# Optimization experiments

Hardware: AMD Instinct MI355X
Metric: run time of the kernel (lower is better)

Reference implementation:

```python
import jax, jax.numpy as jnp
import numpy as np

D_MODEL = 1024
HEADS = 16
Q_DIM = 1024
HEAD_DIM = Q_DIM // HEADS


def setup_inputs() -> dict:
    key = jax.random.key(0)
    ks = jax.random.split(key, 9)
    B, S = 2, 2048
    scale = 1.0 / np.sqrt(D_MODEL)
    inp = {
        "embeddings": jax.random.normal(ks[0], (B, S, D_MODEL), dtype=jnp.float32),
        "Wq": jax.random.normal(ks[1], (D_MODEL, Q_DIM), dtype=jnp.float32) * scale,
        "bq": jnp.zeros((Q_DIM,), dtype=jnp.float32),
        "Wk": jax.random.normal(ks[2], (D_MODEL, Q_DIM), dtype=jnp.float32) * scale,
        "bk": jnp.zeros((Q_DIM,), dtype=jnp.float32),
        "Wv": jax.random.normal(ks[3], (D_MODEL, Q_DIM), dtype=jnp.float32) * scale,
        "bv": jnp.zeros((Q_DIM,), dtype=jnp.float32),
        "Wo": jax.random.normal(ks[4], (Q_DIM, D_MODEL), dtype=jnp.float32) * scale,
        "bo": jnp.zeros((D_MODEL,), dtype=jnp.float32),
    }
    return inp


def reference(embeddings, Wq, bq, Wk, bk, Wv, bv, Wo, bo):
    B, S, _ = embeddings.shape
    # projections -> [B, H, S, Dh]
    def proj(W, b):
        x = embeddings @ W + b
        return x.reshape(B, S, HEADS, HEAD_DIM).transpose(0, 2, 1, 3)
    q = proj(Wq, bq)
    k = proj(Wk, bk)
    v = proj(Wv, bv)
    # scores scaled by sqrt(head_dim) as in source (no mask, dropout is no-op)
    scores = jnp.einsum("bhqd,bhkd->bhqk", q, k) / jnp.sqrt(
        jnp.asarray(HEAD_DIM, dtype=q.dtype)
    )
    p = jax.nn.softmax(scores, axis=-1)
    attn = jnp.einsum("bhqk,bhkd->bhqd", p, v)
    attn = attn.transpose(0, 2, 1, 3).reshape(B, S, Q_DIM)
    return attn @ Wo + bo
```

## Files before the change

### kernel.cpp

```cpp
#include <hip/hip_runtime.h>
#include <hip/hip_bf16.h>

#define BB 2
#define SS 2048
#define DMODEL 1024
#define NHEADS 16
#define DHEAD 64
#define MTOT (BB*SS)
#define NQKV 3072
#define QSCALE 0.18033688011112042f

typedef short bh8 __attribute__((ext_vector_type(8)));
typedef float fx4 __attribute__((ext_vector_type(4)));
typedef unsigned int ux2 __attribute__((ext_vector_type(2)));

__device__ __forceinline__ short f2bs(float f) {
    __hip_bfloat16 h = __float2bfloat16(f);
    return *reinterpret_cast<short*>(&h);
}

__device__ __forceinline__ unsigned pk_bf16(float a, float b) {
    __hip_bfloat162 h = __float22bfloat162_rn(make_float2(a, b));
    return *reinterpret_cast<unsigned*>(&h);
}

__device__ __forceinline__ void gload_lds16(const short* g, short* l) {
    __builtin_amdgcn_global_load_lds(
        (const __attribute__((address_space(1))) unsigned int*)g,
        (__attribute__((address_space(3))) unsigned int*)l, 16, 0, 0);
}

__global__ __launch_bounds__(256) void cvt_emb(const float* __restrict__ x,
                                               short* __restrict__ y, int n) {
    int i = (blockIdx.x * 256 + threadIdx.x) * 4;
    if (i + 3 < n) {
        float4 v = *(const float4*)(x + i);
        short4 o;
        o.x = f2bs(v.x); o.y = f2bs(v.y); o.z = f2bs(v.z); o.w = f2bs(v.w);
        *(short4*)(y + i) = o;
    }
}

__global__ __launch_bounds__(256) void transpose_w(
        const float* __restrict__ Wq, const float* __restrict__ Wk,
        const float* __restrict__ Wv, const float* __restrict__ Wo,
        short* __restrict__ Wt_qkv, short* __restrict__ Wot) {
    __shared__ float tile[64][65];
    int z = blockIdx.z;
    const float* src = (z == 0) ? Wq : (z == 1) ? Wk : (z == 2) ? Wv : Wo;
    short* dst = (z == 3) ? Wot : (Wt_qkv + (size_t)z * 1024 * 1024);
    int n0 = blockIdx.x * 64, k0 = blockIdx.y * 64;
    int tx = threadIdx.x, ty = threadIdx.y;
    for (int j = 0; j < 16; j++) {
        int r = ty + j * 4;
        tile[r][tx] = src[(size_t)(k0 + r) * 1024 + n0 + tx];
    }
    __syncthreads();
    for (int j = 0; j < 16; j++) {
        int r = ty + j * 4;
        dst[(size_t)(n0 + r) * 1024 + k0 + tx] = f2bs(tile[tx][r]);
    }
}

template<int BM, int BN, int NN, int MODE>
__global__ __launch_bounds__(256) void gemm_bt_t(
        const short* __restrict__ A, const short* __restrict__ Bt,
        const float* __restrict__ bq, const float* __restrict__ bk,
        const float* __restrict__ bv, const float* __restrict__ bo,
        short* __restrict__ Qout, short* __restrict__ Kout,
        short* __restrict__ Vtout, float* __restrict__ Cout) {
    const int K = 1024;
    constexpr int ROWS = BM + BN;
    constexpr int CPW  = ROWS / 64;
    constexpr int MBK  = MTOT / BM;
    constexpr int STRIP = MBK / 8;
    constexpr int MT = BM / 32, NT = BN / 32;
    __shared__ __align__(16) short S[3][ROWS * 32];

    int tid = threadIdx.x;
    int w = tid >> 6, l = tid & 63, quad = l >> 4, ln = l & 15;
    int wm = w & 1, wn = w >> 1;

    int id = blockIdx.x;
    int xcd = id & 7, local = id >> 3;
    int mi = xcd * STRIP + (local % STRIP);
    int ni = local / STRIP;
    int m0 = mi * BM, n0 = ni * BN;

    const short* gsrc[CPW];
    int loff[CPW];
    #pragma unroll
    for (int j = 0; j < CPW; j++) {
        int r0 = (w * CPW + j) * 16;
        int row = r0 + (l >> 2);
        gsrc[j] = (r0 < BM ? A + (size_t)(m0 + row) * K
                           : Bt + (size_t)(n0 + row - BM) * K) + (l & 3) * 8;
        loff[j] = r0 * 32;
    }

    short *sC = &S[0][0], *sN = &S[1][0], *sN2 = &S[2][0];
    #pragma unroll
    for (int j = 0; j < CPW; j++) gload_lds16(gsrc[j], sC + loff[j]);
    #pragma unroll
    for (int j = 0; j < CPW; j++) gload_lds16(gsrc[j] + 32, sN + loff[j]);

    fx4 acc[MT][NT] = {};
    for (int it = 0; it < 32; ++it) {
        if (it < 31) {
            if constexpr (CPW == 4)
                asm volatile("s_waitcnt vmcnt(4)\n\ts_barrier" ::: "memory");
            else
                asm volatile("s_waitcnt vmcnt(3)\n\ts_barrier" ::: "memory");
        } else {
            asm volatile("s_waitcnt vmcnt(0)\n\ts_barrier" ::: "memory");
        }
        if (it < 30) {
            int k0 = (it + 2) * 32;
            #pragma unroll
            for (int j = 0; j < CPW; j++) gload_lds16(gsrc[j] + k0, sN2 + loff[j]);
        }
        bh8 af[MT], bf[NT];
        #pragma unroll
        for (int mt = 0; mt < MT; mt++)
            af[mt] = *(const bh8*)&sC[(wm * (BM / 2) + mt * 16 + ln) * 32 + quad * 8];
        #pragma unroll
        for (int nt = 0; nt < NT; nt++)
            bf[nt] = *(const bh8*)&sC[(BM + wn * (BN / 2) + nt * 16 + ln) * 32 + quad * 8];
        #pragma unroll
        for (int mt = 0; mt < MT; mt++)
            #pragma unroll
            for (int nt = 0; nt < NT; nt++)
                acc[mt][nt] = __builtin_amdgcn_mfma_f32_16x16x32_bf16(af[mt], bf[nt], acc[mt][nt], 0, 0, 0);
        short* t;
        t = sC; sC = sN; sN = sN2; sN2 = t;
    }

    #pragma unroll
    for (int mt = 0; mt < MT; mt++) {
        #pragma unroll
        for (int nt = 0; nt < NT; nt++) {
            int n = n0 + wn * (BN / 2) + nt * 16 + ln;
            int mbase = m0 + wm * (BM / 2) + mt * 16 + quad * 4;
            #pragma unroll
            for (int r = 0; r < 4; r++) {
                float v = acc[mt][nt][r];
                int m = mbase + r;
                if constexpr (MODE == 0) {
                    int which = n >> 10, nn = n & 1023, h = nn >> 6, d = nn & 63;
                    float bias = (which == 0) ? bq[nn] : (which == 1) ? bk[nn] : bv[nn];
                    v += bias;
                    int b = m >> 11, s = m & 2047;
                    if (which == 0)
                        Qout[(((size_t)(b * 16 + h) * 2048) + s) * 64 + d] = f2bs(v * QSCALE);
                    else if (which == 1)
                        Kout[(((size_t)(b * 16 + h) * 2048) + s) * 64 + d] = f2bs(v);
                    else
                        Vtout[((size_t)(b * 16 + h) * 64 + d) * 2048 + s] = f2bs(v);
                } else {
                    Cout[(size_t)m * 1024 + n] = v + bo[n];
                }
            }
        }
    }
}

__global__ __launch_bounds__(256, 4) void flash_attn(
        const short* __restrict__ Q, const short* __restrict__ Kg,
        const short* __restrict__ Vt, short* __restrict__ Ctx) {
    __shared__ __align__(16) short SH[16384];

    int tid = threadIdx.x;
    int w = tid >> 6, l = tid & 63, quad = l >> 4, ln = l & 15;
    int id = blockIdx.x;
    int xcd = id & 7, local = id >> 3;
    int bh = xcd * 4 + (local & 3);
    int qx = local >> 2;
    int qblk = qx * 64 + w * 16;
    int b = bh >> 4, h = bh & 15;
    const short* Qb = Q  + (size_t)bh * 2048 * 64;
    const short* Kb = Kg + (size_t)bh * 2048 * 64;
    const short* Vb = Vt + (size_t)bh * 64 * 2048;
    int swz = ln & 7;

    bh8 qf[2];
    #pragma unroll
    for (int c = 0; c < 2; c++)
        qf[c] = *(const bh8*)&Qb[(size_t)(qblk + ln) * 64 + c * 32 + quad * 8];

    const short* srcK[2]; const short* srcV[2]; int dstoff[2];
    #pragma unroll
    for (int j = 0; j < 2; j++) {
        int c = w * 2 + j;
        int row = c * 8 + (l >> 3);
        int pg = (l & 7) ^ (row & 7);
        srcK[j] = Kb + row * 64 + pg * 8;
        srcV[j] = Vb + (size_t)row * 2048 + pg * 8;
        dstoff[j] = c * 512;
    }

    #pragma unroll
    for (int j = 0; j < 2; j++) {
        gload_lds16(srcK[j], SH + dstoff[j]);
        gload_lds16(srcV[j], SH + 8192 + dstoff[j]);
    }

    fx4 o[4] = {};
    float lpart = 0.f;

    for (int it = 0; it < 32; ++it) {
        int koff = (it & 1) ? 4096 : 0;
        asm volatile("s_waitcnt vmcnt(0) lgkmcnt(0)\n\ts_barrier" ::: "memory");
        if (it < 31) {
            int noff = koff ^ 4096;
            int kg = (it + 1) * 4096, vg = (it + 1) * 64;
            #pragma unroll
            for (int j = 0; j < 2; j++) {
                gload_lds16(srcK[j] + kg, SH + noff + dstoff[j]);
                gload_lds16(srcV[j] + vg, SH + 8192 + noff + dstoff[j]);
            }
        }
        const short* ksb = SH + koff;
        const short* vsb = SH + 8192 + koff;

        fx4 s[4] = {};
        #pragma unroll
        for (int mt = 0; mt < 4; mt++) {
            bh8 kf0 = *(const bh8*)&ksb[(mt * 16 + ln) * 64 + ((quad ^ swz) * 8)];
            bh8 kf1 = *(const bh8*)&ksb[(mt * 16 + ln) * 64 + (((quad + 4) ^ swz) * 8)];
            s[mt] = __builtin_amdgcn_mfma_f32_16x16x32_bf16(kf0, qf[0], s[mt], 0, 0, 0);
            s[mt] = __builtin_amdgcn_mfma_f32_16x16x32_bf16(kf1, qf[1], s[mt], 0, 0, 0);
        }

        float e[4][4];
        #pragma unroll
        for (int mt = 0; mt < 4; mt++) {
            #pragma unroll
            for (int r = 0; r < 4; r++)
                e[mt][r] = __builtin_amdgcn_exp2f(s[mt][r]);
            lpart += (e[mt][0] + e[mt][1]) + (e[mt][2] + e[mt][3]);
        }
        bh8 pf[2];
        #pragma unroll
        for (int c2 = 0; c2 < 2; c2++) {
            unsigned xa = pk_bf16(e[2 * c2][0], e[2 * c2][1]);
            unsigned ya = pk_bf16(e[2 * c2][2], e[2 * c2][3]);
            unsigned xb = pk_bf16(e[2 * c2 + 1][0], e[2 * c2 + 1][1]);
            unsigned yb = pk_bf16(e[2 * c2 + 1][2], e[2 * c2 + 1][3]);
            ux2 u  = __builtin_amdgcn_permlane32_swap(xa, xb, false, false);
            ux2 d02 = __builtin_amdgcn_permlane16_swap(u.x, u.y, false, false);
            ux2 u2 = __builtin_amdgcn_permlane32_swap(ya, yb, false, false);
            ux2 d13 = __builtin_amdgcn_permlane16_swap(u2.x, u2.y, false, false);
            union { unsigned u4[4]; bh8 v; } pk_;
            pk_.u4[0] = d02.x; pk_.u4[1] = d13.x;
            pk_.u4[2] = d02.y; pk_.u4[3] = d13.y;
            pf[c2] = pk_.v;
        }

        #pragma unroll
        for (int c2 = 0; c2 < 2; c2++) {
            #pragma unroll
            for (int dt = 0; dt < 4; dt++) {
                bh8 vf = *(const bh8*)&vsb[(dt * 16 + ln) * 64 + (((c2 * 4 + quad) ^ swz) * 8)];
                o[dt] = __builtin_amdgcn_mfma_f32_16x16x32_bf16(vf, pf[c2], o[dt], 0, 0, 0);
            }
        }
    }

    asm volatile("s_waitcnt vmcnt(0) lgkmcnt(0)\n\ts_barrier" ::: "memory");

    float* PsF = (float*)SH + w * 1088;
    int row = l >> 2, seg = l & 3;
    #pragma unroll
    for (int dt = 0; dt < 4; dt++)
        *(fx4*)&PsF[ln * 68 + dt * 16 + quad * 4] = o[dt];
    asm volatile("s_waitcnt lgkmcnt(0)" ::: "memory");
    float lr = lpart;
    lr += __shfl_xor(lr, 16);
    lr += __shfl_xor(lr, 32);
    float invr = __shfl(1.0f / lr, row);
    int q = qblk + row;
    short* crow = Ctx + ((size_t)(b * 2048 + q)) * 1024 + h * 64 + seg * 16;
    union { short s[8]; uint4 u; } o0, o1;
    #pragma unroll
    for (int j = 0; j < 2; j++) {
        fx4 v = *(fx4*)&PsF[row * 68 + seg * 16 + j * 4];
        o0.s[j * 4 + 0] = f2bs(v[0] * invr);
        o0.s[j * 4 + 1] = f2bs(v[1] * invr);
        o0.s[j * 4 + 2] = f2bs(v[2] * invr);
        o0.s[j * 4 + 3] = f2bs(v[3] * invr);
    }
    #pragma unroll
    for (int j = 2; j < 4; j++) {
        fx4 v = *(fx4*)&PsF[row * 68 + seg * 16 + j * 4];
        o1.s[(j - 2) * 4 + 0] = f2bs(v[0] * invr);
        o1.s[(j - 2) * 4 + 1] = f2bs(v[1] * invr);
        o1.s[(j - 2) * 4 + 2] = f2bs(v[2] * invr);
        o1.s[(j - 2) * 4 + 3] = f2bs(v[3] * invr);
    }
    *(uint4*)&crow[0] = o0.u;
    *(uint4*)&crow[8] = o1.u;
}

extern "C" void kernel_launch(void* const* d_in, const int* in_sizes, int n_in,
                              void* d_out, int out_size, void* d_ws, size_t ws_size,
                              hipStream_t stream) {
    const float* emb = (const float*)d_in[0];
    const float* Wq  = (const float*)d_in[1];
    const float* bq  = (const float*)d_in[2];
    const float* Wk  = (const float*)d_in[3];
    const float* bk  = (const float*)d_in[4];
    const float* Wv  = (const float*)d_in[5];
    const float* bv  = (const float*)d_in[6];
    const float* Wo  = (const float*)d_in[7];
    const float* bo  = (const float*)d_in[8];

    char* ws = (char*)d_ws;
    const size_t MB = 1024 * 1024;
    short* Xbf  = (short*)(ws + 0);
    short* Ctx  = (short*)(ws + 0);
    short* Wt   = (short*)(ws + 8 * MB);
    short* Wot  = (short*)(ws + 17 * MB);
    short* Qb   = (short*)(ws + 19 * MB);
    short* Kb   = (short*)(ws + 27 * MB);
    short* Vtb  = (short*)(ws + 35 * MB);

    cvt_emb<<<4096, 256, 0, stream>>>(emb, Xbf, MTOT * DMODEL);
    transpose_w<<<dim3(16, 16, 4), dim3(64, 4), 0, stream>>>(Wq, Wk, Wv, Wo, Wt, Wot);
    gemm_bt_t<128, 128, NQKV, 0><<<768, 256, 0, stream>>>(
        Xbf, Wt, bq, bk, bv, nullptr, Qb, Kb, Vtb, nullptr);
    flash_attn<<<1024, 256, 0, stream>>>(Qb, Kb, Vtb, Ctx);
    gemm_bt_t<64, 128, DMODEL, 1><<<512, 256, 0, stream>>>(
        Ctx, Wot, nullptr, nullptr, nullptr, bo, nullptr, nullptr, nullptr, (float*)d_out);
}
```

Measured before the change: 201.4 us.

## Split attention waves over query and key halves, MFMA row sums, cross-wave reduction

Each wave now handles 32 query rows and half of each 64-key tile (a 2x2 wave split) instead of 16 query rows and the full tile. Each K and V fragment read from LDS therefore feeds two query tiles, roughly halving LDS fragment reads per MFMA. Row sums of the softmax denominator are computed with an MFMA against a ones vector instead of VALU adds, and the MFMA sections are wrapped in s_setprio. At the end the two key-half partial outputs are reduced through LDS with an extra barrier, and only half the waves write the output. This costs more registers and a serial epilogue step.

Result: no change. 198.9 us (-1.2%).

```diff
diff --git a/kernel.cpp b/kernel.cpp
--- a/kernel.cpp
+++ b/kernel.cpp
@@ -171,21 +171,29 @@
 
     int tid = threadIdx.x;
     int w = tid >> 6, l = tid & 63, quad = l >> 4, ln = l & 15;
+    int wq = w & 1, wk = w >> 1;
     int id = blockIdx.x;
     int xcd = id & 7, local = id >> 3;
     int bh = xcd * 4 + (local & 3);
     int qx = local >> 2;
-    int qblk = qx * 64 + w * 16;
+    int qblk = qx * 64 + wq * 32;
     int b = bh >> 4, h = bh & 15;
     const short* Qb = Q  + (size_t)bh * 2048 * 64;
     const short* Kb = Kg + (size_t)bh * 2048 * 64;
     const short* Vb = Vt + (size_t)bh * 64 * 2048;
     int swz = ln & 7;
 
-    bh8 qf[2];
-    #pragma unroll
-    for (int c = 0; c < 2; c++)
-        qf[c] = *(const bh8*)&Qb[(size_t)(qblk + ln) * 64 + c * 32 + quad * 8];
+    bh8 qf[2][2];
+    #pragma unroll
+    for (int qt = 0; qt < 2; qt++)
+        #pragma unroll
+        for (int c = 0; c < 2; c++)
+            qf[qt][c] = *(const bh8*)&Qb[(size_t)(qblk + qt * 16 + ln) * 64 + c * 32 + quad * 8];
+
+    union { short s[8]; bh8 v; } one_;
+    #pragma unroll
+    for (int j = 0; j < 8; j++) one_.s[j] = 0x3F80;
+    bh8 onesv = one_.v;
 
     const short* srcK[2]; const short* srcV[2]; int dstoff[2];
     #pragma unroll
@@ -204,8 +212,8 @@
         gload_lds16(srcV[j], SH + 8192 + dstoff[j]);
     }
 
-    fx4 o[4] = {};
-    float lpart = 0.f;
+    fx4 o[2][4] = {};
+    fx4 lacc[2] = {};
 
     for (int it = 0; it < 32; ++it) {
         int koff = (it & 1) ? 4096 : 0;
@@ -222,83 +230,122 @@
         const short* ksb = SH + koff;
         const short* vsb = SH + 8192 + koff;
 
-        fx4 s[4] = {};
-        #pragma unroll
-        for (int mt = 0; mt < 4; mt++) {
-            bh8 kf0 = *(const bh8*)&ksb[(mt * 16 + ln) * 64 + ((quad ^ swz) * 8)];
-            bh8 kf1 = *(const bh8*)&ksb[(mt * 16 + ln) * 64 + (((quad + 4) ^ swz) * 8)];
-            s[mt] = __builtin_amdgcn_mfma_f32_16x16x32_bf16(kf0, qf[0], s[mt], 0, 0, 0);
-            s[mt] = __builtin_amdgcn_mfma_f32_16x16x32_bf16(kf1, qf[1], s[mt], 0, 0, 0);
-        }
-
-        float e[4][4];
-        #pragma unroll
-        for (int mt = 0; mt < 4; mt++) {
-            #pragma unroll
-            for (int r = 0; r < 4; r++)
-                e[mt][r] = __builtin_amdgcn_exp2f(s[mt][r]);
-            lpart += (e[mt][0] + e[mt][1]) + (e[mt][2] + e[mt][3]);
-        }
+        bh8 kf[2][2];
+        #pragma unroll
+        for (int mt = 0; mt < 2; mt++) {
+            int krow = (wk * 32 + mt * 16 + ln) * 64;
+            kf[mt][0] = *(const bh8*)&ksb[krow + ((quad ^ swz) * 8)];
+            kf[mt][1] = *(const bh8*)&ksb[krow + (((quad + 4) ^ swz) * 8)];
+        }
+        fx4 s[2][2] = {};
+        __builtin_amdgcn_s_setprio(1);
+        #pragma unroll
+        for (int mt = 0; mt < 2; mt++)
+            #pragma unroll
+            for (int qt = 0; qt < 2; qt++) {
+                s[qt][mt] = __builtin_amdgcn_mfma_f32_16x16x32_bf16(kf[mt][0], qf[qt][0], s[qt][mt], 0, 0, 0);
+                s[qt][mt] = __builtin_amdgcn_mfma_f32_16x16x32_bf16(kf[mt][1], qf[qt][1], s[qt][mt], 0, 0, 0);
+            }
+        __builtin_amdgcn_s_setprio(0);
+
         bh8 pf[2];
         #pragma unroll
-        for (int c2 = 0; c2 < 2; c2++) {
-            unsigned xa = pk_bf16(e[2 * c2][0], e[2 * c2][1]);
-            unsigned ya = pk_bf16(e[2 * c2][2], e[2 * c2][3]);
-            unsigned xb = pk_bf16(e[2 * c2 + 1][0], e[2 * c2 + 1][1]);
-            unsigned yb = pk_bf16(e[2 * c2 + 1][2], e[2 * c2 + 1][3]);
-            ux2 u  = __builtin_amdgcn_permlane32_swap(xa, xb, false, false);
+        for (int qt = 0; qt < 2; qt++) {
+            float e0[4], e1[4];
+            #pragma unroll
+            for (int r = 0; r < 4; r++) {
+                e0[r] = __builtin_amdgcn_exp2f(s[qt][0][r]);
+                e1[r] = __builtin_amdgcn_exp2f(s[qt][1][r]);
+            }
+            unsigned xa = pk_bf16(e0[0], e0[1]);
+            unsigned ya = pk_bf16(e0[2], e0[3]);
+            unsigned xb = pk_bf16(e1[0], e1[1]);
+            unsigned yb = pk_bf16(e1[2], e1[3]);
+            ux2 u   = __builtin_amdgcn_permlane32_swap(xa, xb, false, false);
             ux2 d02 = __builtin_amdgcn_permlane16_swap(u.x, u.y, false, false);
-            ux2 u2 = __builtin_amdgcn_permlane32_swap(ya, yb, false, false);
+            ux2 u2  = __builtin_amdgcn_permlane32_swap(ya, yb, false, false);
             ux2 d13 = __builtin_amdgcn_permlane16_swap(u2.x, u2.y, false, false);
             union { unsigned u4[4]; bh8 v; } pk_;
             pk_.u4[0] = d02.x; pk_.u4[1] = d13.x;
             pk_.u4[2] = d02.y; pk_.u4[3] = d13.y;
-            pf[c2] = pk_.v;
-        }
-
-        #pragma unroll
-        for (int c2 = 0; c2 < 2; c2++) {
-            #pragma unroll
-            for (int dt = 0; dt < 4; dt++) {
-                bh8 vf = *(const bh8*)&vsb[(dt * 16 + ln) * 64 + (((c2 * 4 + quad) ^ swz) * 8)];
-                o[dt] = __builtin_amdgcn_mfma_f32_16x16x32_bf16(vf, pf[c2], o[dt], 0, 0, 0);
-            }
-        }
+            pf[qt] = pk_.v;
+        }
+
+        __builtin_amdgcn_s_setprio(1);
+        #pragma unroll
+        for (int dt = 0; dt < 4; dt++) {
+            bh8 vf = *(const bh8*)&vsb[(dt * 16 + ln) * 64 + (((wk * 4 + quad) ^ swz) * 8)];
+            o[0][dt] = __builtin_amdgcn_mfma_f32_16x16x32_bf16(vf, pf[0], o[0][dt], 0, 0, 0);
+            o[1][dt] = __builtin_amdgcn_mfma_f32_16x16x32_bf16(vf, pf[1], o[1][dt], 0, 0, 0);
+        }
+        lacc[0] = __builtin_amdgcn_mfma_f32_16x16x32_bf16(onesv, pf[0], lacc[0], 0, 0, 0);
+        lacc[1] = __builtin_amdgcn_mfma_f32_16x16x32_bf16(onesv, pf[1], lacc[1], 0, 0, 0);
+        __builtin_amdgcn_s_setprio(0);
     }
 
     asm volatile("s_waitcnt vmcnt(0) lgkmcnt(0)\n\ts_barrier" ::: "memory");
 
-    float* PsF = (float*)SH + w * 1088;
-    int row = l >> 2, seg = l & 3;
-    #pragma unroll
-    for (int dt = 0; dt < 4; dt++)
-        *(fx4*)&PsF[ln * 68 + dt * 16 + quad * 4] = o[dt];
-    asm volatile("s_waitcnt lgkmcnt(0)" ::: "memory");
-    float lr = lpart;
-    lr += __shfl_xor(lr, 16);
-    lr += __shfl_xor(lr, 32);
-    float invr = __shfl(1.0f / lr, row);
-    int q = qblk + row;
-    short* crow = Ctx + ((size_t)(b * 2048 + q)) * 1024 + h * 64 + seg * 16;
-    union { short s[8]; uint4 u; } o0, o1;
-    #pragma unroll
-    for (int j = 0; j < 2; j++) {
-        fx4 v = *(fx4*)&PsF[row * 68 + seg * 16 + j * 4];
-        o0.s[j * 4 + 0] = f2bs(v[0] * invr);
-        o0.s[j * 4 + 1] = f2bs(v[1] * invr);
-        o0.s[j * 4 + 2] = f2bs(v[2] * invr);
-        o0.s[j * 4 + 3] = f2bs(v[3] * invr);
-    }
-    #pragma unroll
-    for (int j = 2; j < 4; j++) {
-        fx4 v = *(fx4*)&PsF[row * 68 + seg * 16 + j * 4];
-        o1.s[(j - 2) * 4 + 0] = f2bs(v[0] * invr);
-        o1.s[(j - 2) * 4 + 1] = f2bs(v[1] * invr);
-        o1.s[(j - 2) * 4 + 2] = f2bs(v[2] * invr);
-        o1.s[(j - 2) * 4 + 3] = f2bs(v[3] * invr);
-    }
-    *(uint4*)&crow[0] = o0.u;
-    *(uint4*)&crow[8] = o1.u;
+    float* R  = (float*)SH + 2176;
+    float* R2 = (float*)SH + 2176 + 4096;
+
+    if (wk == 1) {
+        float* Rw = R + wq * 2048;
+        #pragma unroll
+        for (int qt = 0; qt < 2; qt++)
+            #pragma unroll
+            for (int dt = 0; dt < 4; dt++)
+                *(fx4*)&Rw[(((qt * 4 + dt) * 4 + quad) * 16 + ln) * 4] = o[qt][dt];
+        if (quad == 0) {
+            R2[wq * 32 + 0 * 16 + ln] = lacc[0][0];
+            R2[wq * 32 + 1 * 16 + ln] = lacc[1][0];
+        }
+    }
+    asm volatile("s_waitcnt lgkmcnt(0)\n\ts_barrier" ::: "memory");
+
+    if (wk == 0) {
+        float* Rw = R + wq * 2048;
+        float linv[2];
+        #pragma unroll
+        for (int qt = 0; qt < 2; qt++) {
+            #pragma unroll
+            for (int dt = 0; dt < 4; dt++)
+                o[qt][dt] += *(const fx4*)&Rw[(((qt * 4 + dt) * 4 + quad) * 16 + ln) * 4];
+            float lf = lacc[qt][0] + R2[wq * 32 + qt * 16 + ln];
+            linv[qt] = 1.0f / lf;
+        }
+        float* PsF = (float*)SH + wq * 1088;
+        int row = l >> 2, seg = l & 3;
+        #pragma unroll
+        for (int qt = 0; qt < 2; qt++) {
+            #pragma unroll
+            for (int dt = 0; dt < 4; dt++)
+                *(fx4*)&PsF[ln * 68 + dt * 16 + quad * 4] = o[qt][dt];
+            asm volatile("s_waitcnt lgkmcnt(0)" ::: "memory");
+            float invr = __shfl(linv[qt], row);
+            int q = qblk + qt * 16 + row;
+            short* crow = Ctx + ((size_t)(b * 2048 + q)) * 1024 + h * 64 + seg * 16;
+            union { short s[8]; uint4 u; } o0, o1;
+            #pragma unroll
+            for (int j = 0; j < 2; j++) {
+                fx4 v = *(const fx4*)&PsF[row * 68 + seg * 16 + j * 4];
+                o0.s[j * 4 + 0] = f2bs(v[0] * invr);
+                o0.s[j * 4 + 1] = f2bs(v[1] * invr);
+                o0.s[j * 4 + 2] = f2bs(v[2] * invr);
+                o0.s[j * 4 + 3] = f2bs(v[3] * invr);
+            }
+            #pragma unroll
+            for (int j = 2; j < 4; j++) {
+                fx4 v = *(const fx4*)&PsF[row * 68 + seg * 16 + j * 4];
+                o1.s[(j - 2) * 4 + 0] = f2bs(v[0] * invr);
+                o1.s[(j - 2) * 4 + 1] = f2bs(v[1] * invr);
+                o1.s[(j - 2) * 4 + 2] = f2bs(v[2] * invr);
+                o1.s[(j - 2) * 4 + 3] = f2bs(v[3] * invr);
+            }
+            *(uint4*)&crow[0] = o0.u;
+            *(uint4*)&crow[8] = o1.u;
+            asm volatile("s_waitcnt lgkmcnt(0)" ::: "memory");
+        }
+    }
 }
 
 extern "C" void kernel_launch(void* const* d_in, const int* in_sizes, int n_in,
```
